# Kernel tuning notes

Hardware: AMD Instinct MI355X
Metric: run time of the kernel (lower is better)

Reference implementation:

```python
import jax, jax.numpy as jnp
import numpy as np

NUM_GRAPHS = 1024


def setup_inputs() -> dict:
    key = jax.random.key(0)
    k1, k2, k3, k4 = jax.random.split(key, 4)
    N, D, H = 500000, 256, 256
    x = jax.random.normal(k1, (N, D), dtype=jnp.float32)
    batch = jnp.sort(jax.random.randint(k2, (N,), 0, NUM_GRAPHS, dtype=jnp.int64))
    # Linear init scale ~ 1/sqrt(fan_in)
    W1 = jax.random.normal(k3, (D, H), dtype=jnp.float32) / np.sqrt(D)
    b1 = jnp.zeros((H,), dtype=jnp.float32)
    W2 = jax.random.normal(k4, (H, 1), dtype=jnp.float32) / np.sqrt(H)
    b2 = jnp.zeros((1,), dtype=jnp.float32)
    return {"x": x, "batch": batch, "W1": W1, "b1": b1, "W2": W2, "b2": b2}


def reference(x, batch, W1, b1, W2, b2):
    # Two-layer attention MLP -> scores [N, 1] (dropout = identity at eval)
    scores = jnp.tanh(x @ W1 + b1) @ W2 + b2
    # Softmax over dim 0 (global over all nodes, as in the source)
    attn = jax.nn.softmax(scores, axis=0)  # [N, 1]
    # Weighted scatter-add pooling per graph id
    pooled = jax.ops.segment_sum(x * attn, batch, num_segments=NUM_GRAPHS)
    return pooled  # [NUM_GRAPHS, D]
```

## Files before the change

kernel.cpp:

```cpp
#include <hip/hip_runtime.h>
#include <stdint.h>

#define NBLOCKS 256
#define TROWS 64
#define SMEM_BYTES (131072 + TROWS * 512)

typedef __attribute__((ext_vector_type(8))) short bfrag_t;
typedef __attribute__((ext_vector_type(4))) float f32x4;
typedef __attribute__((ext_vector_type(2))) unsigned int u32x2;

static __device__ __forceinline__ unsigned short f2bf(float f) {
  unsigned int u = __float_as_uint(f);
  u += 0x7fffu + ((u >> 16) & 1u);
  return (unsigned short)(u >> 16);
}

static __device__ __forceinline__ float tanh_fast(float s) {
  float e = __builtin_exp2f(s * 2.8853900817779268f);
  float r = __builtin_amdgcn_rcpf(1.f + e);
  return __builtin_fmaf(-2.f, r, 1.f);
}

static __device__ __forceinline__ float readlane_f(float v, int l) {
  return __uint_as_float(__builtin_amdgcn_readlane(__float_as_uint(v), l));
}

static __device__ __forceinline__ bfrag_t pack8(f32x4 a, f32x4 b) {
  union { bfrag_t v; unsigned int u[4]; } r;
  asm("v_cvt_pk_bf16_f32 %0, %1, %2" : "=v"(r.u[0]) : "v"(a[0]), "v"(a[1]));
  asm("v_cvt_pk_bf16_f32 %0, %1, %2" : "=v"(r.u[1]) : "v"(a[2]), "v"(a[3]));
  asm("v_cvt_pk_bf16_f32 %0, %1, %2" : "=v"(r.u[2]) : "v"(b[0]), "v"(b[1]));
  asm("v_cvt_pk_bf16_f32 %0, %1, %2" : "=v"(r.u[3]) : "v"(b[2]), "v"(b[3]));
  return r.v;
}

#define GLD16(gp, lp) __builtin_amdgcn_global_load_lds( \
    (const __attribute__((address_space(1))) void*)(gp), \
    (__attribute__((address_space(3))) void*)(lp), 16, 0, 0)

__global__ void prep_w1_kernel(const float* __restrict__ W1, unsigned short* __restrict__ W1f) {
  const int bx = blockIdx.x;
  const int l = threadIdx.x;
  const int cc = bx >> 3, kk = bx & 7;
  const int h = cc * 16 + (l & 15);
  const int kbase = kk * 32 + ((l >> 4) << 3);
  bfrag_t pk;
#pragma unroll
  for (int j = 0; j < 8; ++j) pk[j] = (short)f2bf(W1[(size_t)(kbase + j) * 256 + h]);
  *(bfrag_t*)(W1f + (size_t)(bx * 64 + l) * 8) = pk;
}

__attribute__((amdgpu_flat_work_group_size(256, 256), amdgpu_waves_per_eu(1, 1)))
__global__ void attnpool_kernel(const float* __restrict__ x,
                                const int* __restrict__ batch,
                                const unsigned short* __restrict__ W1f,
                                const float* __restrict__ b1,
                                const float* __restrict__ W2,
                                const float* __restrict__ b2,
                                float* __restrict__ out,
                                float* __restrict__ Zp,
                                int N, int base, int rem) {
  extern __shared__ char smem[];
  char* Bl = smem;
  char* xt = smem + 131072;

  const int t = threadIdx.x;
  const int lane = t & 63;
  const int wv = t >> 6;
  const int l15 = lane & 15;
  const int hi = lane >> 4;

  const int blk = blockIdx.x;
  const int cnt = base + (blk < rem ? 1 : 0);
  const int tile0 = blk * base + min(blk, rem);

#pragma unroll
  for (int i = 0; i < 32; ++i) {
    const int f = wv * 32 + i;
    GLD16(W1f + (size_t)f * 512 + lane * 8, Bl + f * 1024);
  }

  float b1v[16], w2v[16];
#pragma unroll
  for (int cc = 0; cc < 16; ++cc) {
    b1v[cc] = b1[cc * 16 + l15];
    w2v[cc] = W2[cc * 16 + l15];
  }
  const float b2c = b2[0];

  const int srow = t >> 5;
  const int soct = t & 31;
  f32x4 sreg[16];
  auto issue_loads = [&](int tile) {
#pragma unroll
    for (int p = 0; p < 8; ++p) {
      const int row = p * 8 + srow;
      const int rg = min(tile * TROWS + row, N - 1);
      const float* s = x + (size_t)rg * 256 + soct * 8;
      sreg[2 * p] = *(const f32x4*)s;
      sreg[2 * p + 1] = *(const f32x4*)(s + 4);
    }
  };
  auto write_tile = [&]() {
#pragma unroll
    for (int p = 0; p < 8; ++p) {
      const int row = p * 8 + srow;
      *(bfrag_t*)(xt + row * 512 + ((soct * 16) ^ ((row & 7) << 4))) =
          pack8(sreg[2 * p], sreg[2 * p + 1]);
    }
  };

  issue_loads(tile0);
  write_tile();
  __syncthreads();

  float zacc = 0.f;
  f32x4 pacc = {0.f, 0.f, 0.f, 0.f};
  int gcur = -1;

  auto flush = [&]() {
    float* po = out + (size_t)gcur * 256 + lane * 4;
    atomicAdd(po + 0, pacc[0]); atomicAdd(po + 1, pacc[1]);
    atomicAdd(po + 2, pacc[2]); atomicAdd(po + 3, pacc[3]);
    pacc[0] = pacc[1] = pacc[2] = pacc[3] = 0.f;
  };

  for (int tt = 0; tt < cnt; ++tt) {
    const int tile = tile0 + tt;
    const int R0 = tile * TROWS;

    if (tt + 1 < cnt) issue_loads(tile + 1);

    bfrag_t A0[8];
    {
      const int arow = wv * 16 + l15;
      const int sw = (l15 & 7) << 4;
      const char* ap = xt + arow * 512;
#pragma unroll
      for (int kk = 0; kk < 8; ++kk)
        A0[kk] = *(const bfrag_t*)(ap + ((kk * 64 + hi * 16) ^ sw));
    }

    float s0v[4] = {0.f, 0.f, 0.f, 0.f};
#pragma unroll
    for (int cc = 0; cc < 16; ++cc) {
      f32x4 acc = {0.f, 0.f, 0.f, 0.f};
#pragma unroll
      for (int kk = 0; kk < 8; ++kk) {
        const bfrag_t Bk = *(const bfrag_t*)(Bl + (cc * 8 + kk) * 1024 + lane * 16);
        acc = __builtin_amdgcn_mfma_f32_16x16x32_bf16(A0[kk], Bk, acc, 0, 0, 0);
      }
#pragma unroll
      for (int r = 0; r < 4; ++r)
        s0v[r] += tanh_fast(acc[r] + b1v[cc]) * w2v[cc];
    }

    f32x4 w0v;
#pragma unroll
    for (int r = 0; r < 4; ++r) {
      float v = s0v[r];
      v += __shfl_xor(v, 1); v += __shfl_xor(v, 2);
      v += __shfl_xor(v, 4); v += __shfl_xor(v, 8);
      w0v[r] = (R0 + wv * 16 + hi * 4 + r < N) ? __expf(v + b2c) : 0.f;
    }
    {
      float z = w0v[0] + w0v[1] + w0v[2] + w0v[3];
      z += __shfl_xor(z, 16);
      z += __shfl_xor(z, 32);
      zacc += z;
    }

    float wlane;
    {
      const int rq = lane & 3;
      const float ca = (rq == 0) ? w0v[0] : w0v[1];
      const float cb = (rq == 2) ? w0v[2] : w0v[3];
      const float c = (rq < 2) ? ca : cb;
      const int srcl = (((lane >> 2) & 3) << 4) + rq;
      wlane = __shfl(c, srcl);
    }

    int bid = batch[min(R0 + wv * 16 + l15, N - 1)];

    const int g_first = __builtin_amdgcn_readlane(bid, 0);
    const int g_last = __builtin_amdgcn_readlane(bid, 15);
    if (g_first != gcur) { if (gcur >= 0) flush(); gcur = g_first; }
    const int rowb = wv * 16;
    if (g_first == g_last) {
#pragma unroll
      for (int r = 0; r < 16; ++r) {
        const float wr = readlane_f(wlane, r);
        const int row = rowb + r;
        const u32x2 v = *(const u32x2*)(xt + row * 512 + ((lane * 8) ^ ((row & 7) << 4)));
        pacc[0] = __builtin_fmaf(wr, __uint_as_float(v[0] << 16), pacc[0]);
        pacc[1] = __builtin_fmaf(wr, __uint_as_float(v[0] & 0xffff0000u), pacc[1]);
        pacc[2] = __builtin_fmaf(wr, __uint_as_float(v[1] << 16), pacc[2]);
        pacc[3] = __builtin_fmaf(wr, __uint_as_float(v[1] & 0xffff0000u), pacc[3]);
      }
    } else {
      for (int r = 0; r < 16; ++r) {
        const int g = __builtin_amdgcn_readlane(bid, r);
        if (g != gcur) { flush(); gcur = g; }
        const float wr = readlane_f(wlane, r);
        const int row = rowb + r;
        const u32x2 v = *(const u32x2*)(xt + row * 512 + ((lane * 8) ^ ((row & 7) << 4)));
        pacc[0] = __builtin_fmaf(wr, __uint_as_float(v[0] << 16), pacc[0]);
        pacc[1] = __builtin_fmaf(wr, __uint_as_float(v[0] & 0xffff0000u), pacc[1]);
        pacc[2] = __builtin_fmaf(wr, __uint_as_float(v[1] << 16), pacc[2]);
        pacc[3] = __builtin_fmaf(wr, __uint_as_float(v[1] & 0xffff0000u), pacc[3]);
      }
    }

    __syncthreads();
    if (tt + 1 < cnt) write_tile();
    __syncthreads();
  }

  if (gcur >= 0) flush();
  if (lane == 0 && zacc != 0.f) atomicAdd(Zp, zacc);
}

__global__ void finalize_kernel(float* __restrict__ out, const float* __restrict__ Zp, int n4) {
  const int i = blockIdx.x * blockDim.x + threadIdx.x;
  if (i < n4) {
    const float zi = 1.f / Zp[0];
    f32x4* p = (f32x4*)out;
    f32x4 v = p[i];
    v[0] *= zi; v[1] *= zi; v[2] *= zi; v[3] *= zi;
    p[i] = v;
  }
}

extern "C" void kernel_launch(void* const* d_in, const int* in_sizes, int n_in,
                              void* d_out, int out_size, void* d_ws, size_t ws_size,
                              hipStream_t stream) {
  const float* x  = (const float*)d_in[0];
  const int* batch = (const int*)d_in[1];
  const float* W1 = (const float*)d_in[2];
  const float* b1 = (const float*)d_in[3];
  const float* W2 = (const float*)d_in[4];
  const float* b2 = (const float*)d_in[5];
  float* out = (float*)d_out;
  const int N = in_sizes[1];

  unsigned short* W1f = (unsigned short*)d_ws;
  float* Zp = (float*)((char*)d_ws + 131072);

  static int attr_done = 0;
  if (!attr_done) {
    hipFuncSetAttribute((const void*)attnpool_kernel,
                        hipFuncAttributeMaxDynamicSharedMemorySize, SMEM_BYTES);
    attr_done = 1;
  }

  const int ntiles = (N + TROWS - 1) / TROWS;
  const int base = ntiles / NBLOCKS;
  const int rem = ntiles % NBLOCKS;

  hipMemsetAsync(d_out, 0, (size_t)out_size * sizeof(float), stream);
  hipMemsetAsync(Zp, 0, sizeof(float), stream);
  prep_w1_kernel<<<128, 64, 0, stream>>>(W1, W1f);
  attnpool_kernel<<<NBLOCKS, 256, SMEM_BYTES, stream>>>(x, batch, W1f, b1, W2, b2,
                                                        out, Zp, N, base, rem);
  finalize_kernel<<<(out_size / 4 + 255) / 256, 256, 0, stream>>>(out, Zp, out_size / 4);
}
```

Before: 192.1 us.

## Split hidden dimension across two wave groups with 512-thread blocks

```diff
diff --git a/kernel.cpp b/kernel.cpp
--- a/kernel.cpp
+++ b/kernel.cpp
@@ -3,7 +3,10 @@
 
 #define NBLOCKS 256
 #define TROWS 64
-#define SMEM_BYTES (131072 + TROWS * 512)
+#define B_FRAGS 127
+#define XT_OFF (B_FRAGS * 1024)
+#define SPART_OFF (XT_OFF + TROWS * 512)
+#define SMEM_BYTES (SPART_OFF + 512)
 
 typedef __attribute__((ext_vector_type(8))) short bfrag_t;
 typedef __attribute__((ext_vector_type(4))) float f32x4;
@@ -50,7 +53,7 @@
   *(bfrag_t*)(W1f + (size_t)(bx * 64 + l) * 8) = pk;
 }
 
-__attribute__((amdgpu_flat_work_group_size(256, 256), amdgpu_waves_per_eu(1, 1)))
+__attribute__((amdgpu_flat_work_group_size(512, 512), amdgpu_waves_per_eu(2, 2)))
 __global__ void attnpool_kernel(const float* __restrict__ x,
                                 const int* __restrict__ batch,
                                 const unsigned short* __restrict__ W1f,
@@ -62,11 +65,14 @@
                                 int N, int base, int rem) {
   extern __shared__ char smem[];
   char* Bl = smem;
-  char* xt = smem + 131072;
+  char* xt = smem + XT_OFF;
+  float* spart = (float*)(smem + SPART_OFF);
 
   const int t = threadIdx.x;
   const int lane = t & 63;
   const int wv = t >> 6;
+  const int rg = wv & 3;
+  const int cg = wv >> 2;
   const int l15 = lane & 15;
   const int hi = lane >> 4;
 
@@ -75,36 +81,36 @@
   const int tile0 = blk * base + min(blk, rem);
 
 #pragma unroll
-  for (int i = 0; i < 32; ++i) {
-    const int f = wv * 32 + i;
-    GLD16(W1f + (size_t)f * 512 + lane * 8, Bl + f * 1024);
-  }
-
-  float b1v[16], w2v[16];
-#pragma unroll
-  for (int cc = 0; cc < 16; ++cc) {
-    b1v[cc] = b1[cc * 16 + l15];
-    w2v[cc] = W2[cc * 16 + l15];
+  for (int i = 0; i < 16; ++i) {
+    const int f = wv * 16 + i;
+    if (f < B_FRAGS) GLD16(W1f + (size_t)f * 512 + lane * 8, Bl + f * 1024);
+  }
+
+  float b1v[8], w2v[8];
+#pragma unroll
+  for (int i = 0; i < 8; ++i) {
+    b1v[i] = b1[(cg * 8 + i) * 16 + l15];
+    w2v[i] = W2[(cg * 8 + i) * 16 + l15];
   }
   const float b2c = b2[0];
 
   const int srow = t >> 5;
   const int soct = t & 31;
-  f32x4 sreg[16];
+  f32x4 sreg[8];
   auto issue_loads = [&](int tile) {
 #pragma unroll
-    for (int p = 0; p < 8; ++p) {
-      const int row = p * 8 + srow;
-      const int rg = min(tile * TROWS + row, N - 1);
-      const float* s = x + (size_t)rg * 256 + soct * 8;
+    for (int p = 0; p < 4; ++p) {
+      const int row = p * 16 + srow;
+      const int rgb = min(tile * TROWS + row, N - 1);
+      const float* s = x + (size_t)rgb * 256 + soct * 8;
       sreg[2 * p] = *(const f32x4*)s;
       sreg[2 * p + 1] = *(const f32x4*)(s + 4);
     }
   };
   auto write_tile = [&]() {
 #pragma unroll
-    for (int p = 0; p < 8; ++p) {
-      const int row = p * 8 + srow;
+    for (int p = 0; p < 4; ++p) {
+      const int row = p * 16 + srow;
       *(bfrag_t*)(xt + row * 512 + ((soct * 16) ^ ((row & 7) << 4))) =
           pack8(sreg[2 * p], sreg[2 * p + 1]);
     }
@@ -133,7 +139,7 @@
 
     bfrag_t A0[8];
     {
-      const int arow = wv * 16 + l15;
+      const int arow = rg * 16 + l15;
       const int sw = (l15 & 7) << 4;
       const char* ap = xt + arow * 512;
 #pragma unroll
@@ -143,27 +149,46 @@
 
     float s0v[4] = {0.f, 0.f, 0.f, 0.f};
 #pragma unroll
-    for (int cc = 0; cc < 16; ++cc) {
+    for (int i = 0; i < 8; ++i) {
+      const int cc = cg * 8 + i;
       f32x4 acc = {0.f, 0.f, 0.f, 0.f};
 #pragma unroll
       for (int kk = 0; kk < 8; ++kk) {
-        const bfrag_t Bk = *(const bfrag_t*)(Bl + (cc * 8 + kk) * 1024 + lane * 16);
+        const int frag = cc * 8 + kk;
+        bfrag_t Bk;
+        if (frag == B_FRAGS)
+          Bk = *(const bfrag_t*)(W1f + (size_t)frag * 512 + lane * 8);
+        else
+          Bk = *(const bfrag_t*)(Bl + frag * 1024 + lane * 16);
         acc = __builtin_amdgcn_mfma_f32_16x16x32_bf16(A0[kk], Bk, acc, 0, 0, 0);
       }
 #pragma unroll
       for (int r = 0; r < 4; ++r)
-        s0v[r] += tanh_fast(acc[r] + b1v[cc]) * w2v[cc];
-    }
-
-    f32x4 w0v;
+        s0v[r] += tanh_fast(acc[r] + b1v[i]) * w2v[i];
+    }
+
 #pragma unroll
     for (int r = 0; r < 4; ++r) {
       float v = s0v[r];
       v += __shfl_xor(v, 1); v += __shfl_xor(v, 2);
       v += __shfl_xor(v, 4); v += __shfl_xor(v, 8);
-      w0v[r] = (R0 + wv * 16 + hi * 4 + r < N) ? __expf(v + b2c) : 0.f;
-    }
-    {
+      s0v[r] = v;
+    }
+    if (l15 == 0) {
+#pragma unroll
+      for (int r = 0; r < 4; ++r)
+        spart[cg * 64 + rg * 16 + hi * 4 + r] = s0v[r];
+    }
+    __syncthreads();
+
+    f32x4 w0v;
+#pragma unroll
+    for (int r = 0; r < 4; ++r) {
+      const int row = rg * 16 + hi * 4 + r;
+      const float s = s0v[r] + spart[(cg ^ 1) * 64 + row] + b2c;
+      w0v[r] = (R0 + row < N) ? __expf(s) : 0.f;
+    }
+    if (cg == 0) {
       float z = w0v[0] + w0v[1] + w0v[2] + w0v[3];
       z += __shfl_xor(z, 16);
       z += __shfl_xor(z, 32);
@@ -180,16 +205,16 @@
       wlane = __shfl(c, srcl);
     }
 
-    int bid = batch[min(R0 + wv * 16 + l15, N - 1)];
-
-    const int g_first = __builtin_amdgcn_readlane(bid, 0);
-    const int g_last = __builtin_amdgcn_readlane(bid, 15);
+    int bid = batch[min(R0 + rg * 16 + l15, N - 1)];
+
+    const int g_first = __builtin_amdgcn_readlane(bid, cg * 8);
+    const int g_last = __builtin_amdgcn_readlane(bid, cg * 8 + 7);
     if (g_first != gcur) { if (gcur >= 0) flush(); gcur = g_first; }
-    const int rowb = wv * 16;
+    const int rowb = rg * 16 + cg * 8;
     if (g_first == g_last) {
 #pragma unroll
-      for (int r = 0; r < 16; ++r) {
-        const float wr = readlane_f(wlane, r);
+      for (int r = 0; r < 8; ++r) {
+        const float wr = readlane_f(wlane, cg * 8 + r);
         const int row = rowb + r;
         const u32x2 v = *(const u32x2*)(xt + row * 512 + ((lane * 8) ^ ((row & 7) << 4)));
         pacc[0] = __builtin_fmaf(wr, __uint_as_float(v[0] << 16), pacc[0]);
@@ -198,10 +223,10 @@
         pacc[3] = __builtin_fmaf(wr, __uint_as_float(v[1] & 0xffff0000u), pacc[3]);
       }
     } else {
-      for (int r = 0; r < 16; ++r) {
-        const int g = __builtin_amdgcn_readlane(bid, r);
+      for (int r = 0; r < 8; ++r) {
+        const int g = __builtin_amdgcn_readlane(bid, cg * 8 + r);
         if (g != gcur) { flush(); gcur = g; }
-        const float wr = readlane_f(wlane, r);
+        const float wr = readlane_f(wlane, cg * 8 + r);
         const int row = rowb + r;
         const u32x2 v = *(const u32x2*)(xt + row * 512 + ((lane * 8) ^ ((row & 7) << 4)));
         pacc[0] = __builtin_fmaf(wr, __uint_as_float(v[0] << 16), pacc[0]);
@@ -260,7 +285,7 @@
   hipMemsetAsync(d_out, 0, (size_t)out_size * sizeof(float), stream);
   hipMemsetAsync(Zp, 0, sizeof(float), stream);
   prep_w1_kernel<<<128, 64, 0, stream>>>(W1, W1f);
-  attnpool_kernel<<<NBLOCKS, 256, SMEM_BYTES, stream>>>(x, batch, W1f, b1, W2, b2,
+  attnpool_kernel<<<NBLOCKS, 512, SMEM_BYTES, stream>>>(x, batch, W1f, b1, W2, b2,
                                                         out, Zp, N, base, rem);
   finalize_kernel<<<(out_size / 4 + 255) / 256, 256, 0, stream>>>(out, Zp, out_size / 4);
 }
```

Result: faster. 178.9 us (-6.9%).

## Make each wave independent: per-wave tiles, direct global loads, W1 from cache

Applied to the files above, without the earlier changes.

```diff
diff --git a/kernel.cpp b/kernel.cpp
--- a/kernel.cpp
+++ b/kernel.cpp
@@ -1,9 +1,12 @@
 #include <hip/hip_runtime.h>
 #include <stdint.h>
 
-#define NBLOCKS 256
-#define TROWS 64
-#define SMEM_BYTES (131072 + TROWS * 512)
+#define NBLOCKS 1024
+#define WPB 4
+#define SLOTS (NBLOCKS * WPB)
+#define TR 16
+#define LDSW 8192
+#define SMEM_BYTES (WPB * LDSW)
 
 typedef __attribute__((ext_vector_type(8))) short bfrag_t;
 typedef __attribute__((ext_vector_type(4))) float f32x4;
@@ -34,9 +37,8 @@
   return r.v;
 }
 
-#define GLD16(gp, lp) __builtin_amdgcn_global_load_lds( \
-    (const __attribute__((address_space(1))) void*)(gp), \
-    (__attribute__((address_space(3))) void*)(lp), 16, 0, 0)
+#define KEEPA(A) asm volatile("" : "+v"(A[0]), "+v"(A[1]), "+v"(A[2]), "+v"(A[3]), \
+                                    "+v"(A[4]), "+v"(A[5]), "+v"(A[6]), "+v"(A[7]))
 
 __global__ void prep_w1_kernel(const float* __restrict__ W1, unsigned short* __restrict__ W1f) {
   const int bx = blockIdx.x;
@@ -50,7 +52,7 @@
   *(bfrag_t*)(W1f + (size_t)(bx * 64 + l) * 8) = pk;
 }
 
-__attribute__((amdgpu_flat_work_group_size(256, 256), amdgpu_waves_per_eu(1, 1)))
+__launch_bounds__(256, 4)
 __global__ void attnpool_kernel(const float* __restrict__ x,
                                 const int* __restrict__ batch,
                                 const unsigned short* __restrict__ W1f,
@@ -61,24 +63,17 @@
                                 float* __restrict__ Zp,
                                 int N, int base, int rem) {
   extern __shared__ char smem[];
-  char* Bl = smem;
-  char* xt = smem + 131072;
-
   const int t = threadIdx.x;
   const int lane = t & 63;
   const int wv = t >> 6;
   const int l15 = lane & 15;
   const int hi = lane >> 4;
 
-  const int blk = blockIdx.x;
-  const int cnt = base + (blk < rem ? 1 : 0);
-  const int tile0 = blk * base + min(blk, rem);
-
-#pragma unroll
-  for (int i = 0; i < 32; ++i) {
-    const int f = wv * 32 + i;
-    GLD16(W1f + (size_t)f * 512 + lane * 8, Bl + f * 1024);
-  }
+  char* xb = smem + wv * LDSW;
+
+  const int slot = blockIdx.x * WPB + wv;
+  const int cnt = base + (slot < rem ? 1 : 0);
+  const int tile0 = slot * base + min(slot, rem);
 
   float b1v[16], w2v[16];
 #pragma unroll
@@ -87,32 +82,7 @@
     w2v[cc] = W2[cc * 16 + l15];
   }
   const float b2c = b2[0];
-
-  const int srow = t >> 5;
-  const int soct = t & 31;
-  f32x4 sreg[16];
-  auto issue_loads = [&](int tile) {
-#pragma unroll
-    for (int p = 0; p < 8; ++p) {
-      const int row = p * 8 + srow;
-      const int rg = min(tile * TROWS + row, N - 1);
-      const float* s = x + (size_t)rg * 256 + soct * 8;
-      sreg[2 * p] = *(const f32x4*)s;
-      sreg[2 * p + 1] = *(const f32x4*)(s + 4);
-    }
-  };
-  auto write_tile = [&]() {
-#pragma unroll
-    for (int p = 0; p < 8; ++p) {
-      const int row = p * 8 + srow;
-      *(bfrag_t*)(xt + row * 512 + ((soct * 16) ^ ((row & 7) << 4))) =
-          pack8(sreg[2 * p], sreg[2 * p + 1]);
-    }
-  };
-
-  issue_loads(tile0);
-  write_tile();
-  __syncthreads();
+  const bfrag_t* Wf = (const bfrag_t*)W1f;
 
   float zacc = 0.f;
   f32x4 pacc = {0.f, 0.f, 0.f, 0.f};
@@ -127,27 +97,36 @@
 
   for (int tt = 0; tt < cnt; ++tt) {
     const int tile = tile0 + tt;
-    const int R0 = tile * TROWS;
-
-    if (tt + 1 < cnt) issue_loads(tile + 1);
+    const int R0 = tile * TR;
+
+    int bid = batch[R0 + l15];
 
     bfrag_t A0[8];
     {
-      const int arow = wv * 16 + l15;
+      const float* p0 = x + (size_t)(R0 + l15) * 256 + hi * 8;
+#pragma unroll
+      for (int kk = 0; kk < 8; ++kk) {
+        const f32x4 u0 = *(const f32x4*)(p0 + kk * 32);
+        const f32x4 u1 = *(const f32x4*)(p0 + kk * 32 + 4);
+        A0[kk] = pack8(u0, u1);
+      }
+    }
+
+    {
       const int sw = (l15 & 7) << 4;
-      const char* ap = xt + arow * 512;
 #pragma unroll
       for (int kk = 0; kk < 8; ++kk)
-        A0[kk] = *(const bfrag_t*)(ap + ((kk * 64 + hi * 16) ^ sw));
+        *(bfrag_t*)(xb + l15 * 512 + ((kk * 64 + hi * 16) ^ sw)) = A0[kk];
     }
 
     float s0v[4] = {0.f, 0.f, 0.f, 0.f};
-#pragma unroll
+#pragma unroll 2
     for (int cc = 0; cc < 16; ++cc) {
+      KEEPA(A0);
       f32x4 acc = {0.f, 0.f, 0.f, 0.f};
 #pragma unroll
       for (int kk = 0; kk < 8; ++kk) {
-        const bfrag_t Bk = *(const bfrag_t*)(Bl + (cc * 8 + kk) * 1024 + lane * 16);
+        const bfrag_t Bk = Wf[(cc * 8 + kk) * 64 + lane];
         acc = __builtin_amdgcn_mfma_f32_16x16x32_bf16(A0[kk], Bk, acc, 0, 0, 0);
       }
 #pragma unroll
@@ -161,10 +140,10 @@
       float v = s0v[r];
       v += __shfl_xor(v, 1); v += __shfl_xor(v, 2);
       v += __shfl_xor(v, 4); v += __shfl_xor(v, 8);
-      w0v[r] = (R0 + wv * 16 + hi * 4 + r < N) ? __expf(v + b2c) : 0.f;
-    }
-    {
-      float z = w0v[0] + w0v[1] + w0v[2] + w0v[3];
+      w0v[r] = __expf(v + b2c);
+    }
+    {
+      float z = (l15 == 0) ? (w0v[0] + w0v[1] + w0v[2] + w0v[3]) : 0.f;
       z += __shfl_xor(z, 16);
       z += __shfl_xor(z, 32);
       zacc += z;
@@ -180,40 +159,31 @@
       wlane = __shfl(c, srcl);
     }
 
-    int bid = batch[min(R0 + wv * 16 + l15, N - 1)];
-
     const int g_first = __builtin_amdgcn_readlane(bid, 0);
     const int g_last = __builtin_amdgcn_readlane(bid, 15);
     if (g_first != gcur) { if (gcur >= 0) flush(); gcur = g_first; }
-    const int rowb = wv * 16;
     if (g_first == g_last) {
 #pragma unroll
-      for (int r = 0; r < 16; ++r) {
+      for (int r = 0; r < TR; ++r) {
         const float wr = readlane_f(wlane, r);
-        const int row = rowb + r;
-        const u32x2 v = *(const u32x2*)(xt + row * 512 + ((lane * 8) ^ ((row & 7) << 4)));
+        const u32x2 v = *(const u32x2*)(xb + r * 512 + ((lane * 8) ^ ((r & 7) << 4)));
         pacc[0] = __builtin_fmaf(wr, __uint_as_float(v[0] << 16), pacc[0]);
         pacc[1] = __builtin_fmaf(wr, __uint_as_float(v[0] & 0xffff0000u), pacc[1]);
         pacc[2] = __builtin_fmaf(wr, __uint_as_float(v[1] << 16), pacc[2]);
         pacc[3] = __builtin_fmaf(wr, __uint_as_float(v[1] & 0xffff0000u), pacc[3]);
       }
     } else {
-      for (int r = 0; r < 16; ++r) {
+      for (int r = 0; r < TR; ++r) {
         const int g = __builtin_amdgcn_readlane(bid, r);
         if (g != gcur) { flush(); gcur = g; }
         const float wr = readlane_f(wlane, r);
-        const int row = rowb + r;
-        const u32x2 v = *(const u32x2*)(xt + row * 512 + ((lane * 8) ^ ((row & 7) << 4)));
+        const u32x2 v = *(const u32x2*)(xb + r * 512 + ((lane * 8) ^ ((r & 7) << 4)));
         pacc[0] = __builtin_fmaf(wr, __uint_as_float(v[0] << 16), pacc[0]);
         pacc[1] = __builtin_fmaf(wr, __uint_as_float(v[0] & 0xffff0000u), pacc[1]);
         pacc[2] = __builtin_fmaf(wr, __uint_as_float(v[1] << 16), pacc[2]);
         pacc[3] = __builtin_fmaf(wr, __uint_as_float(v[1] & 0xffff0000u), pacc[3]);
       }
     }
-
-    __syncthreads();
-    if (tt + 1 < cnt) write_tile();
-    __syncthreads();
   }
 
   if (gcur >= 0) flush();
@@ -253,9 +223,9 @@
     attr_done = 1;
   }
 
-  const int ntiles = (N + TROWS - 1) / TROWS;
-  const int base = ntiles / NBLOCKS;
-  const int rem = ntiles % NBLOCKS;
+  const int ntiles = (N + TR - 1) / TR;
+  const int base = ntiles / SLOTS;
+  const int rem = ntiles % SLOTS;
 
   hipMemsetAsync(d_out, 0, (size_t)out_size * sizeof(float), stream);
   hipMemsetAsync(Zp, 0, sizeof(float), stream);
```

After: 367.3 us. 91.2% more time.
